# Kernel optimization log

Measured on AMD Instinct MI355X. Metric: run time of the kernel, lower is better.

Reference implementation:

```python
import jax, jax.numpy as jnp
import numpy as np

D, L, W, K = 16, 1000000, 64, 8
PAD = (W - 1) // 2  # 31, matches padding1 in the torch code


def setup_inputs() -> dict:
    key = jax.random.key(0)
    kx, kp = jax.random.split(key)
    x = jax.random.normal(kx, (D, L), dtype=jnp.float32)
    # torch uses torch.rand (uniform [0,1)) for each of the K (D,W) parameters
    P = jax.random.uniform(kp, (K, D, W), dtype=jnp.float32)
    return {"x": x, "P": P}


def _fullscan(x, P):
    # x: (D, L); P: (K, D, W)
    p = PAD
    # --- middle positions k in [p, L-W+p]: standard valid correlation ---
    # mid[k_out, o] = sum_{d,m} x[d, o+m] * P[k_out, d, m], position k = o + p
    mid = jax.lax.conv_general_dilated(
        x[None],                      # (1, D, L)
        P,                            # (K, D, W)
        window_strides=(1,),
        padding="VALID",
        dimension_numbers=("NCH", "OIH", "NCH"),
    )[0]                              # (K, L-W+1)
    # --- left edge k in [0, p): data x[:, :k+W-p] * kernel[:, :k+W-p] ---
    # prefix[i, m] = sum_d x[d, m] * P[i, d, m] over the first W samples
    tl = jnp.einsum("dm,kdm->km", x[:, :W], P)        # (K, W)
    left_c = jnp.cumsum(tl, axis=1)                    # prefix sums
    left = left_c[:, W - p - 1 : W - 1]                # (K, p)
    # --- right edge k in (L-W+p, L): data x[:, k-p:] * kernel[:, W+k-L-p:] ---
    tr = jnp.einsum("dm,kdm->km", x[:, L - W :], P)    # (K, W)
    suf = jnp.cumsum(tr[:, ::-1], axis=1)[:, ::-1]     # suffix sums: suf[:, t] = sum_{m>=t}
    right = suf[:, 1 : W - p]                          # (K, W-1-p)
    y = jnp.concatenate([left, mid, right], axis=1)    # (K, L)
    return y.reshape(-1, 1)                            # (K*L, 1)


def reference(x, P):
    return _fullscan(x, P)
```

## Files before the change

kernel.cpp:

```cpp
#include <hip/hip_runtime.h>


constexpr int D    = 16;
constexpr int L    = 1000000;
constexpr int W    = 64;
constexpr int K    = 8;
constexpr int PADL = 31;
constexpr int NMID = L - W + 1;
constexpr int TPB  = 256;
constexpr int OTW  = 4;
constexpr int CTW  = OTW + 2;
constexpr int BLK_OUT = 4 * OTW * 32;
constexpr int XS   = 592;
constexpr int NBLK = (NMID + BLK_OUT - 1) / BLK_OUT;
constexpr int NGRID = NBLK + K;

typedef __attribute__((ext_vector_type(8)))  short short8;
typedef __attribute__((ext_vector_type(16))) float floatx16;

__device__ __forceinline__ unsigned short f2bf(float f) {
    union { float f; unsigned u; } v; v.f = f;
    unsigned u = v.u + 0x7fff + ((v.u >> 16) & 1);
    return (unsigned short)(u >> 16);
}

__global__ __launch_bounds__(TPB, 4) void fullscan_mid(
    const float* __restrict__ x, const float* __restrict__ P,
    const unsigned short* __restrict__ afr, float* __restrict__ out)
{
    __shared__ __align__(16) unsigned short xs[XS * 16];
    const int bid = blockIdx.x;
    const int tid = threadIdx.x;

    if (bid >= NBLK) {
        const int k = bid - NBLK;
        const int j = tid;
        if (j < PADL) {
            float acc = 0.0f;
            for (int m = 0; m <= 32 + j; ++m)
#pragma unroll
                for (int d = 0; d < D; ++d)
                    acc = fmaf(x[d * L + m], P[(k * D + d) * W + m], acc);
            out[k * L + j] = acc;
        } else if (j < 2 * PADL + 1) {
            const int jj = j - PADL;
            float acc = 0.0f;
            for (int m = jj + 1; m < W; ++m)
#pragma unroll
                for (int d = 0; d < D; ++d)
                    acc = fmaf(x[d * L + (L - W) + m], P[(k * D + d) * W + m], acc);
            out[k * L + PADL + NMID + jj] = acc;
        }
        return;
    }

    const int s0   = bid * BLK_OUT;
    const int lane = tid & 63;
    const int wv   = tid >> 6;

    short8 A[16];
#pragma unroll
    for (int c = 0; c < 16; ++c)
        A[c] = *(const short8*)(afr + (c * 64 + lane) * 8);

    {
        const int pl = tid & 63;
        const int dq = tid >> 6;
        const float* xr0 = x + (4 * dq + 0) * L + s0;
        const float* xr1 = x + (4 * dq + 1) * L + s0;
        const float* xr2 = x + (4 * dq + 2) * L + s0;
        const float* xr3 = x + (4 * dq + 3) * L + s0;
#pragma unroll 2
        for (int b = 0; b < XS; b += 64) {
            const int pos = b + pl;
            if (pos < XS) {
                const bool ok = (s0 + pos) < L;
                const float v0 = ok ? xr0[pos] : 0.0f;
                const float v1 = ok ? xr1[pos] : 0.0f;
                const float v2 = ok ? xr2[pos] : 0.0f;
                const float v3 = ok ? xr3[pos] : 0.0f;
                unsigned long long w =
                    (unsigned long long)f2bf(v0)
                  | ((unsigned long long)f2bf(v1) << 16)
                  | ((unsigned long long)f2bf(v2) << 32)
                  | ((unsigned long long)f2bf(v3) << 48);
                const int swz = (pos >> 2) & 1;
                *(unsigned long long*)&xs[pos * 16 + ((dq * 4) ^ (swz * 8))] = w;
            }
        }
    }
    __syncthreads();

    const int n  = lane & 31;
    const int h  = lane >> 5;
    const int hb = h * 8;
    const int wbase = wv * OTW;

    float pendA[4], pendB[4], prev4[4], prev12[4];

#pragma unroll
    for (int jj = 0; jj < CTW; ++jj) {
        floatx16 acc;
#pragma unroll
        for (int r = 0; r < 16; ++r) acc[r] = 0.0f;
        const int p0 = (wbase + jj) * 32 + n;

        short8 Bf[3];
#pragma unroll
        for (int c = 0; c < 3; ++c) {
            const int pos = p0 + c;
            Bf[c] = *(const short8*)
                &xs[pos * 16 + (hb ^ (((pos >> 2) & 1) * 8))];
        }
#pragma unroll
        for (int c = 0; c < 16; ++c) {
            acc = __builtin_amdgcn_mfma_f32_32x32x16_bf16(A[c], Bf[c % 3], acc, 0, 0, 0);
            if (c + 3 < 16) {
                const int pos = p0 + c + 3;
                Bf[c % 3] = *(const short8*)
                    &xs[pos * 16 + (hb ^ (((pos >> 2) & 1) * 8))];
            }
        }

        if (jj >= 2) {
            const int ot = jj - 2;
            const int t = s0 + (wbase + ot) * 32 + n;
#pragma unroll
            for (int kk = 0; kk < 4; ++kk) {
                const float g3t = (n >= 16) ? prev12[kk] : acc[kk + 12];
                const float v = pendA[kk] + __shfl_xor(g3t, 16, 64);
                if (t < NMID)
                    out[(kk + 4 * h) * L + PADL + t] = v;
            }
        }
        if (jj >= 1) {
#pragma unroll
            for (int kk = 0; kk < 4; ++kk) {
                const float g1t = (n >= 16) ? prev4[kk] : acc[kk + 4];
                pendA[kk] = pendB[kk] + acc[kk + 8] + __shfl_xor(g1t, 16, 64);
            }
        }
#pragma unroll
        for (int kk = 0; kk < 4; ++kk) {
            pendB[kk]  = acc[kk];
            prev4[kk]  = acc[kk + 4];
            prev12[kk] = acc[kk + 12];
        }
    }
}

__global__ void fullscan_prep(const float* __restrict__ P,
                              unsigned short* __restrict__ afr)
{
    const int u = blockIdx.x * 256 + threadIdx.x;
    const int c = u >> 9, lane = (u >> 3) & 63, j = u & 7;
    const int m = lane & 31, h = lane >> 5;
    const int k = m & 7, g = m >> 3;
    const int d = 8 * h + j;
    const int w = 16 * g + c;
    afr[u] = f2bf(P[(k * D + d) * W + w]);
}

extern "C" void kernel_launch(void* const* d_in, const int* in_sizes, int n_in,
                              void* d_out, int out_size, void* d_ws, size_t ws_size,
                              hipStream_t stream)
{
    const float* x = (const float*)d_in[0];
    const float* P = (const float*)d_in[1];
    float* out = (float*)d_out;
    unsigned short* afr = (unsigned short*)d_ws;

    hipLaunchKernelGGL(fullscan_prep, dim3(32), dim3(256), 0, stream, P, afr);
    hipLaunchKernelGGL(fullscan_mid, dim3(NGRID), dim3(TPB), 0, stream,
                       x, P, afr, out);
}
```

Before: 151.0 us.

## Stage x as fp32 via direct global-to-LDS loads, convert to bf16 per MFMA

New measurement: 159.2 us. +5.5%, slower.

```diff
diff --git a/kernel.cpp b/kernel.cpp
--- a/kernel.cpp
+++ b/kernel.cpp
@@ -12,6 +12,8 @@
 constexpr int CTW  = OTW + 2;
 constexpr int BLK_OUT = 4 * OTW * 32;
 constexpr int XS   = 592;
+constexpr int SROWS = XS / 4;
+constexpr int SPW  = SROWS / 4;
 constexpr int NBLK = (NMID + BLK_OUT - 1) / BLK_OUT;
 constexpr int NGRID = NBLK + K;
 
@@ -24,11 +26,11 @@
     return (unsigned short)(u >> 16);
 }
 
-__global__ __launch_bounds__(TPB, 4) void fullscan_mid(
+__global__ __launch_bounds__(TPB, 3) void fullscan_mid(
     const float* __restrict__ x, const float* __restrict__ P,
     const unsigned short* __restrict__ afr, float* __restrict__ out)
 {
-    __shared__ __align__(16) unsigned short xs[XS * 16];
+    __shared__ __align__(16) float xs32[XS * 16];
     const int bid = blockIdx.x;
     const int tid = threadIdx.x;
 
@@ -58,43 +60,43 @@
     const int lane = tid & 63;
     const int wv   = tid >> 6;
 
+    {
+        const int rof = lane >> 4;
+        const int dsw = 4 * (((lane >> 2) & 3) ^ rof) + (lane & 3);
+        if (s0 + XS <= L) {
+            typedef const __attribute__((address_space(1))) float gfloat;
+            typedef __attribute__((address_space(3))) float lfloat;
+            gfloat* gp = (gfloat*)(x + (size_t)dsw * L + s0 + rof
+                                     + (size_t)wv * (SPW * 4));
+            lfloat* lp = (lfloat*)(xs32 + wv * (SPW * 64));
+#pragma unroll
+            for (int j = 0; j < SPW; ++j)
+                __builtin_amdgcn_global_load_lds(gp + j * 4, lp + j * 64, 4, 0, 0);
+        } else {
+#pragma unroll 1
+            for (int i = 0; i < (XS * 16) / TPB; ++i) {
+                const int Wd = i * TPB + tid;
+                const int r  = Wd >> 4, w = Wd & 15;
+                const int d  = 4 * ((w >> 2) ^ (r & 3)) + (w & 3);
+                const int pos = s0 + r;
+                xs32[Wd] = (pos < L) ? x[(size_t)d * L + pos] : 0.0f;
+            }
+        }
+    }
+
     short8 A[16];
 #pragma unroll
     for (int c = 0; c < 16; ++c)
         A[c] = *(const short8*)(afr + (c * 64 + lane) * 8);
 
-    {
-        const int pl = tid & 63;
-        const int dq = tid >> 6;
-        const float* xr0 = x + (4 * dq + 0) * L + s0;
-        const float* xr1 = x + (4 * dq + 1) * L + s0;
-        const float* xr2 = x + (4 * dq + 2) * L + s0;
-        const float* xr3 = x + (4 * dq + 3) * L + s0;
-#pragma unroll 2
-        for (int b = 0; b < XS; b += 64) {
-            const int pos = b + pl;
-            if (pos < XS) {
-                const bool ok = (s0 + pos) < L;
-                const float v0 = ok ? xr0[pos] : 0.0f;
-                const float v1 = ok ? xr1[pos] : 0.0f;
-                const float v2 = ok ? xr2[pos] : 0.0f;
-                const float v3 = ok ? xr3[pos] : 0.0f;
-                unsigned long long w =
-                    (unsigned long long)f2bf(v0)
-                  | ((unsigned long long)f2bf(v1) << 16)
-                  | ((unsigned long long)f2bf(v2) << 32)
-                  | ((unsigned long long)f2bf(v3) << 48);
-                const int swz = (pos >> 2) & 1;
-                *(unsigned long long*)&xs[pos * 16 + ((dq * 4) ^ (swz * 8))] = w;
-            }
-        }
-    }
     __syncthreads();
 
     const int n  = lane & 31;
     const int h  = lane >> 5;
-    const int hb = h * 8;
     const int wbase = wv * OTW;
+
+#define LD_LO(pos) (*(const float4*)&xs32[(pos) * 16 + ((((2 * h)) ^ ((pos) & 3)) << 2)])
+#define LD_HI(pos) (*(const float4*)&xs32[(pos) * 16 + ((((2 * h + 1)) ^ ((pos) & 3)) << 2)])
 
     float pendA[4], pendB[4], prev4[4], prev12[4];
 
@@ -105,21 +107,18 @@
         for (int r = 0; r < 16; ++r) acc[r] = 0.0f;
         const int p0 = (wbase + jj) * 32 + n;
 
-        short8 Bf[3];
-#pragma unroll
-        for (int c = 0; c < 3; ++c) {
-            const int pos = p0 + c;
-            Bf[c] = *(const short8*)
-                &xs[pos * 16 + (hb ^ (((pos >> 2) & 1) * 8))];
-        }
+        float4 lo = LD_LO(p0), hi = LD_HI(p0);
 #pragma unroll
         for (int c = 0; c < 16; ++c) {
-            acc = __builtin_amdgcn_mfma_f32_32x32x16_bf16(A[c], Bf[c % 3], acc, 0, 0, 0);
-            if (c + 3 < 16) {
-                const int pos = p0 + c + 3;
-                Bf[c % 3] = *(const short8*)
-                    &xs[pos * 16 + (hb ^ (((pos >> 2) & 1) * 8))];
-            }
+            float4 lo_n, hi_n;
+            if (c < 15) { lo_n = LD_LO(p0 + c + 1); hi_n = LD_HI(p0 + c + 1); }
+            short8 B;
+            B[0] = (short)f2bf(lo.x); B[1] = (short)f2bf(lo.y);
+            B[2] = (short)f2bf(lo.z); B[3] = (short)f2bf(lo.w);
+            B[4] = (short)f2bf(hi.x); B[5] = (short)f2bf(hi.y);
+            B[6] = (short)f2bf(hi.z); B[7] = (short)f2bf(hi.w);
+            acc = __builtin_amdgcn_mfma_f32_32x32x16_bf16(A[c], B, acc, 0, 0, 0);
+            lo = lo_n; hi = hi_n;
         }
 
         if (jj >= 2) {
@@ -147,6 +146,8 @@
             prev12[kk] = acc[kk + 12];
         }
     }
+#undef LD_LO
+#undef LD_HI
 }
 
 __global__ void fullscan_prep(const float* __restrict__ P,
```
